# Kernel tuning notes

Measured on AMD Instinct MI355X. Metric: run time of the kernel, lower is better.

## Reference

```python
import jax, jax.numpy as jnp
import numpy as np
import math

MAX_DELAY = 25
TAU = 2.0
VTH = 1.0
BN_EPS = 1e-5
ATAN_ALPHA = 2.0


def build_dcls_kernel(W, P, SIG, D):
    # Gaussian-interpolated DCLS kernel ('gauss' version).
    # W, P, SIG: (O, I, K) -> kernel (O, I, D)
    lim = D // 2
    j = jnp.arange(D, dtype=W.dtype)                      # (D,)
    Pc = jnp.clip(P, -lim, lim) + lim                     # (O, I, K)
    sig = jnp.abs(SIG) + 0.27
    g = jnp.exp(-0.5 * ((j - Pc[..., None]) / sig[..., None]) ** 2)  # (O,I,K,D)
    g = g / (g.sum(-1, keepdims=True) + 1e-7)
    return jnp.einsum('oik,oikd->oid', W, g)


def dcls_conv_positive(x, W, P, SIG, D):
    # Dale-positive: abs(weight) before kernel construction; padding=0 (VALID)
    k = build_dcls_kernel(jnp.abs(W), P, SIG, D)
    return jax.lax.conv_general_dilated(
        x, k, window_strides=(1,), padding='VALID',
        dimension_numbers=('NCW', 'OIW', 'NCW'))


def batchnorm_m(x, gamma, beta):
    # spikingjelly layer.BatchNorm1d step_mode='m' on (T, B, C):
    # flattens (T*B) as batch, normalizes per channel (training-mode stats).
    mean = x.mean(axis=(0, 1))
    var = x.var(axis=(0, 1))
    return (x - mean) * jax.lax.rsqrt(var + BN_EPS) * gamma + beta


def lif_multistep(x_seq, tau, v_th):
    # LIFNode, decay_input=False, v_reset=0 (hard reset), detach_reset=True,
    # ATan surrogate. x_seq: (T, B, C).
    inv_tau = jnp.asarray(1.0 / tau, x_seq.dtype)
    def step(v, xt):
        v = v * (1.0 - inv_tau) + xt              # charge (decay_input=False)
        u = v - v_th
        sg = jnp.arctan(0.5 * math.pi * ATAN_ALPHA * u) / math.pi + 0.5
        hard = (u >= 0).astype(xt.dtype)
        spike = sg + jax.lax.stop_gradient(hard - sg)
        v = v * (1.0 - jax.lax.stop_gradient(spike))   # hard reset, detached
        return v, spike
    v0 = jnp.zeros(x_seq.shape[1:], x_seq.dtype)
    _, spikes = jax.lax.scan(step, v0, x_seq)
    return spikes


def setup_inputs() -> dict:
    key = jax.random.key(0)
    ks = jax.random.split(key, 8)
    B, C_in, T = 64, 700, 300
    n_out, n_inh, K = 256, 128, 1
    return {
        'x': jax.random.normal(ks[0], (B, C_in, T), jnp.float32),
        'W_inh': jax.random.normal(ks[1], (n_inh, C_in, K), jnp.float32),
        'P_inh': jax.random.normal(ks[2], (n_inh, C_in, K), jnp.float32),
        'SIG_inh': jax.random.uniform(ks[3], (n_inh, C_in, K), jnp.float32),
        'W_exc': jax.random.normal(ks[4], (n_out, C_in, K), jnp.float32),
        'P_exc': jax.random.normal(ks[5], (n_out, C_in, K), jnp.float32),
        'SIG_exc': jax.random.uniform(ks[6], (n_out, C_in, K), jnp.float32),
        'w_exc_inh': jax.random.uniform(ks[7], (n_out, n_inh), jnp.float32),
        'bn_gamma': jnp.ones((n_inh,), jnp.float32),
        'bn_beta': jnp.zeros((n_inh,), jnp.float32),
    }


def reference(x, W_inh, P_inh, SIG_inh, W_exc, P_exc, SIG_exc, w_exc_inh,
              bn_gamma, bn_beta):
    # inhibitory branch
    in_inhib = dcls_conv_positive(x, W_inh, P_inh, SIG_inh, MAX_DELAY)  # (B,Ci,T')
    in_inhib = jnp.transpose(in_inhib, (2, 0, 1))                       # (T',B,Ci)
    in_inhib = batchnorm_m(in_inhib, bn_gamma, bn_beta)
    spikes = lif_multistep(in_inhib, TAU, VTH)                          # (T',B,Ci)
    out_inhib = jnp.einsum('tbi,oi->tbo', spikes, -jnp.abs(w_exc_inh))
    out_inhib = jnp.transpose(out_inhib, (1, 2, 0))                     # (B,O,T')
    # excitatory branch
    excit = dcls_conv_positive(x, W_exc, P_exc, SIG_exc, MAX_DELAY)     # (B,O,T')
    return excit + out_inhib
```

## Files before the change

### kernel.cpp

```cpp
#include <hip/hip_runtime.h>
#include <math.h>

#define CI   700
#define TIN  300
#define DD   25
#define TOUT 276
#define BB   64
#define OINH 128
#define OEXC 256

#define TROWS 312
#define IPAD  704

typedef __attribute__((ext_vector_type(8))) short short8;
typedef __attribute__((ext_vector_type(4))) float f32x4;
typedef __attribute__((ext_vector_type(8))) unsigned short ushort8v;

static __device__ __forceinline__ unsigned short f2bf(float f) {
    unsigned int u = __float_as_uint(f);
    unsigned int r = (u + 0x7FFFu + ((u >> 16) & 1u)) >> 16;
    return (unsigned short)r;
}
static __device__ __forceinline__ float bf2f(unsigned short h) {
    return __uint_as_float(((unsigned int)h) << 16);
}

static __device__ __forceinline__ void gload_lds16(const void* g, void* l) {
    __builtin_amdgcn_global_load_lds(
        (const __attribute__((address_space(1))) unsigned int*)g,
        (__attribute__((address_space(3))) unsigned int*)l, 16, 0, 0);
}

__global__ void build_kt(const float* __restrict__ W, const float* __restrict__ P,
                         const float* __restrict__ SIG, float* __restrict__ kt, int O) {
    int n = blockIdx.x * 256 + threadIdx.x;
    if (n >= O * CI) return;
    int o = n % O;
    int i = n / O;
    float w   = fabsf(W[o * CI + i]);
    float p   = fminf(fmaxf(P[o * CI + i], -12.f), 12.f) + 12.f;
    float sig = fabsf(SIG[o * CI + i]) + 0.27f;
    float inv = 1.f / sig;
    float g[DD];
    float sum = 0.f;
#pragma unroll
    for (int d = 0; d < DD; ++d) {
        float e = ((float)d - p) * inv;
        g[d] = expf(-0.5f * e * e);
        sum += g[d];
    }
    float sc = w / (sum + 1e-7f);
#pragma unroll
    for (int d = 0; d < DD; ++d)
        kt[(i * DD + d) * O + o] = g[d] * sc;
}

__global__ void kexc_build(const float* __restrict__ W, const float* __restrict__ P,
                           const float* __restrict__ SIG, unsigned short* __restrict__ kb2) {
    int n = blockIdx.x * 256 + threadIdx.x;
    if (n >= OEXC * IPAD) return;
    int o = n / IPAD, ip = n % IPAD;
    if (ip >= CI) {
#pragma unroll
        for (int d = 0; d < DD; ++d)
            kb2[((size_t)d * OEXC + o) * IPAD + ip] = 0;
        return;
    }
    float w   = fabsf(W[o * CI + ip]);
    float p   = fminf(fmaxf(P[o * CI + ip], -12.f), 12.f) + 12.f;
    float sig = fabsf(SIG[o * CI + ip]) + 0.27f;
    float inv = 1.f / sig;
    float g[DD];
    float sum = 0.f;
#pragma unroll
    for (int d = 0; d < DD; ++d) {
        float e = ((float)d - p) * inv;
        g[d] = expf(-0.5f * e * e);
        sum += g[d];
    }
    float sc = w / (sum + 1e-7f);
#pragma unroll
    for (int d = 0; d < DD; ++d)
        kb2[((size_t)d * OEXC + o) * IPAD + ip] = f2bf(g[d] * sc);
}

__global__ void kinh_build(const float* __restrict__ W, const float* __restrict__ P,
                           const float* __restrict__ SIG,
                           unsigned short* __restrict__ kbh, unsigned short* __restrict__ kbl) {
    int n = blockIdx.x * 256 + threadIdx.x;
    if (n >= OINH * IPAD) return;
    int o = n / IPAD, ip = n % IPAD;
    if (ip >= CI) {
#pragma unroll
        for (int d = 0; d < DD; ++d) {
            kbh[((size_t)d * OINH + o) * IPAD + ip] = 0;
            kbl[((size_t)d * OINH + o) * IPAD + ip] = 0;
        }
        return;
    }
    float w   = fabsf(W[o * CI + ip]);
    float p   = fminf(fmaxf(P[o * CI + ip], -12.f), 12.f) + 12.f;
    float sig = fabsf(SIG[o * CI + ip]) + 0.27f;
    float inv = 1.f / sig;
    float g[DD];
    float sum = 0.f;
#pragma unroll
    for (int d = 0; d < DD; ++d) {
        float e = ((float)d - p) * inv;
        g[d] = expf(-0.5f * e * e);
        sum += g[d];
    }
    float sc = w / (sum + 1e-7f);
#pragma unroll
    for (int d = 0; d < DD; ++d) {
        float v = g[d] * sc;
        unsigned short h = f2bf(v);
        kbh[((size_t)d * OINH + o) * IPAD + ip] = h;
        kbl[((size_t)d * OINH + o) * IPAD + ip] = f2bf(v - bf2f(h));
    }
}

__global__ __launch_bounds__(256)
void xt_kernel(const float* __restrict__ x, unsigned short* __restrict__ xTh,
               unsigned short* __restrict__ xTl) {
    __shared__ float tile[64][65];
    const int tid = threadIdx.x;
    const int t0 = blockIdx.x * 64, i0 = blockIdx.y * 64, b = blockIdx.z;
#pragma unroll
    for (int s = 0; s < 16; ++s) {
        int f = s * 256 + tid;
        int tt = f & 63, ii = f >> 6;
        float v = 0.f;
        if (t0 + tt < TIN && i0 + ii < CI)
            v = x[((size_t)b * CI + i0 + ii) * TIN + t0 + tt];
        tile[tt][ii] = v;
    }
    __syncthreads();
#pragma unroll
    for (int s = 0; s < 2; ++s) {
        int f = s * 256 + tid;
        int tt = f >> 3, g = f & 7;
        if (t0 + tt < TROWS) {
            ushort8v vh, vl;
#pragma unroll
            for (int e = 0; e < 8; ++e) {
                float v = tile[tt][g * 8 + e];
                unsigned short h = f2bf(v);
                vh[e] = h;
                vl[e] = f2bf(v - bf2f(h));
            }
            size_t off = ((size_t)b * TROWS + t0 + tt) * IPAD + i0 + g * 8;
            *(ushort8v*)(xTh + off) = vh;
            if (xTl) *(ushort8v*)(xTl + off) = vl;
        }
    }
}

__global__ void wt_kernel(const float* __restrict__ w, float* __restrict__ wt) {
    int n = blockIdx.x * 256 + threadIdx.x;
    if (n >= OINH * OEXC) return;
    int o = n % OEXC, c = n / OEXC;
    wt[c * OEXC + o] = -fabsf(w[o * OINH + c]);
}

__global__ __launch_bounds__(256)
void conv_fused_v6(const unsigned short* __restrict__ xTh, const unsigned short* __restrict__ xTl,
                   const unsigned short* __restrict__ kb2,
                   const unsigned short* __restrict__ kbh, const unsigned short* __restrict__ kbl,
                   float* __restrict__ pexc0, float* __restrict__ pexc1,
                   float* __restrict__ pinh0, float* __restrict__ pinh1) {
    __shared__ unsigned short lds[16384];

    const int tid  = threadIdx.x;
    const int wave = tid >> 6;
    const int lane = tid & 63;
    const int wo   = wave & 1;
    const int wt2  = wave >> 1;
    const int wtb  = wt2 * 48;
    const int l15 = lane & 15, l4 = lane >> 4;
    const int tt   = blockIdx.x % 3;
    const int ksp  = blockIdx.x / 3;
    const int role = blockIdx.y;
    const int b    = blockIdx.z;
    const int t0   = tt * 96;
    const int icb  = ksp * 11;

    const int ld_r = lane >> 2;
    const int ld_c = (((lane & 3) ^ ((lane >> 3) & 3)) << 4);
    const int SA   = (l15 >> 1) & 3;

    const size_t xstride = (size_t)IPAD * 2;
    const char* xh_base = (const char*)xTh + ((size_t)b * TROWS + t0) * xstride;
    const char* xl_base = (const char*)xTl + ((size_t)b * TROWS + t0) * xstride;

    if (role < 2) {
        unsigned short* xs = lds;
        unsigned short* ks = lds + 4096;
        const int o0 = role * 128;
        const int o0w = o0 + wo * 64;

        f32x4 acc[4][3];
#pragma unroll
        for (int i = 0; i < 4; ++i)
#pragma unroll
            for (int j = 0; j < 3; ++j) acc[i][j] = (f32x4)0.f;

        for (int c = 0; c < 11; ++c) {
            const size_t cb = (size_t)(icb + c) * 64;
            __syncthreads();
            for (int j = wave; j < 8; j += 4)
                gload_lds16(xh_base + (size_t)(16 * j + ld_r) * xstride + cb + ld_c,
                            (char*)xs + j * 1024);
            {
                const char* kbase = (const char*)kb2 + (size_t)o0w * xstride + cb;
                char* kdst = (char*)(ks + (0 * 2 + wo) * 2048);
#pragma unroll
                for (int j = 0; j < 4; ++j)
                    gload_lds16(kbase + (size_t)(16 * j + ld_r) * xstride + ld_c,
                                kdst + j * 1024);
            }
            asm volatile("s_waitcnt vmcnt(0)" ::: "memory");
            __syncthreads();

            for (int d = 0; d < DD; ++d) {
                const int cur = d & 1;
                if (d < DD - 1) {
                    const char* kbase = (const char*)kb2 +
                        ((size_t)((d + 1) * OEXC) + o0w) * xstride + cb;
                    char* kdst = (char*)(ks + ((cur ^ 1) * 2 + wo) * 2048);
#pragma unroll
                    for (int j = 0; j < 4; ++j)
                        gload_lds16(kbase + (size_t)(16 * j + ld_r) * xstride + ld_c,
                                    kdst + j * 1024);
                }
                const char* kp = (const char*)(ks + (cur * 2 + wo) * 2048);
                short8 A[4];
#pragma unroll
                for (int i = 0; i < 4; ++i)
                    A[i] = *(const short8*)(kp + (i * 16 + l15) * 64 + ((l4 ^ SA) << 4));
#pragma unroll
                for (int j = 0; j < 3; ++j) {
                    const int tr = wtb + j * 16 + l15 + d;
                    short8 Bv = *(const short8*)((const char*)xs + tr * 64 +
                                                 ((l4 ^ ((tr >> 1) & 3)) << 4));
#pragma unroll
                    for (int i = 0; i < 4; ++i)
                        acc[i][j] = __builtin_amdgcn_mfma_f32_16x16x32_bf16(
                            A[i], Bv, acc[i][j], 0, 0, 0);
                }
                asm volatile("s_waitcnt vmcnt(0)" ::: "memory");
                __syncthreads();
            }
        }
        float* dst = ksp ? pexc1 : pexc0;
#pragma unroll
        for (int i = 0; i < 4; ++i)
#pragma unroll
            for (int j = 0; j < 3; ++j) {
                const int t = t0 + wtb + j * 16 + l15;
                if (t < TOUT) {
                    float* op = dst + ((size_t)b * OEXC + o0w + i * 16 + l4 * 4) * TOUT + t;
#pragma unroll
                    for (int r = 0; r < 4; ++r) op[(size_t)r * TOUT] = acc[i][j][r];
                }
            }
    } else {
        unsigned short* xsh = lds;
        unsigned short* xsl = lds + 4096;
        unsigned short* kws = lds + 8192;
        const int o0  = (role - 2) * 64;
        const int o0w = o0 + wo * 32;

        f32x4 acc[2][3];
#pragma unroll
        for (int i = 0; i < 2; ++i)
#pragma unroll
            for (int j = 0; j < 3; ++j) acc[i][j] = (f32x4)0.f;

        for (int c = 0; c < 11; ++c) {
            const size_t cb = (size_t)(icb + c) * 64;
            __syncthreads();
            for (int j = wave; j < 8; j += 4) {
                gload_lds16(xh_base + (size_t)(16 * j + ld_r) * xstride + cb + ld_c,
                            (char*)xsh + j * 1024);
                gload_lds16(xl_base + (size_t)(16 * j + ld_r) * xstride + cb + ld_c,
                            (char*)xsl + j * 1024);
            }
            {
                const size_t ko = (size_t)o0w * xstride + cb;
                char* kdst = (char*)(kws + (0 * 2 + wo) * 2048);
#pragma unroll
                for (int j = 0; j < 2; ++j) {
                    gload_lds16((const char*)kbh + ko + (size_t)(16 * j + ld_r) * xstride + ld_c,
                                kdst + j * 1024);
                    gload_lds16((const char*)kbl + ko + (size_t)(16 * j + ld_r) * xstride + ld_c,
                                kdst + 2048 + j * 1024);
                }
            }
            asm volatile("s_waitcnt vmcnt(0)" ::: "memory");
            __syncthreads();

            for (int d = 0; d < DD; ++d) {
                const int cur = d & 1;
                if (d < DD - 1) {
                    const size_t ko = ((size_t)((d + 1) * OINH) + o0w) * xstride + cb;
                    char* kdst = (char*)(kws + ((cur ^ 1) * 2 + wo) * 2048);
#pragma unroll
                    for (int j = 0; j < 2; ++j) {
                        gload_lds16((const char*)kbh + ko + (size_t)(16 * j + ld_r) * xstride + ld_c,
                                    kdst + j * 1024);
                        gload_lds16((const char*)kbl + ko + (size_t)(16 * j + ld_r) * xstride + ld_c,
                                    kdst + 2048 + j * 1024);
                    }
                }
                const char* kp = (const char*)(kws + (cur * 2 + wo) * 2048);
                short8 Ah[2], Al[2];
#pragma unroll
                for (int i = 0; i < 2; ++i) {
                    Ah[i] = *(const short8*)(kp + (i * 16 + l15) * 64 + ((l4 ^ SA) << 4));
                    Al[i] = *(const short8*)(kp + 2048 + (i * 16 + l15) * 64 + ((l4 ^ SA) << 4));
                }
#pragma unroll
                for (int j = 0; j < 3; ++j) {
                    const int tr = wtb + j * 16 + l15 + d;
                    const int xo = tr * 64 + ((l4 ^ ((tr >> 1) & 3)) << 4);
                    short8 Bh = *(const short8*)((const char*)xsh + xo);
                    short8 Bl = *(const short8*)((const char*)xsl + xo);
#pragma unroll
                    for (int i = 0; i < 2; ++i) {
                        acc[i][j] = __builtin_amdgcn_mfma_f32_16x16x32_bf16(
                            Ah[i], Bh, acc[i][j], 0, 0, 0);
                        acc[i][j] = __builtin_amdgcn_mfma_f32_16x16x32_bf16(
                            Ah[i], Bl, acc[i][j], 0, 0, 0);
                        acc[i][j] = __builtin_amdgcn_mfma_f32_16x16x32_bf16(
                            Al[i], Bh, acc[i][j], 0, 0, 0);
                    }
                }
                asm volatile("s_waitcnt vmcnt(0)" ::: "memory");
                __syncthreads();
            }
        }
        float* dst = ksp ? pinh1 : pinh0;
#pragma unroll
        for (int i = 0; i < 2; ++i)
#pragma unroll
            for (int j = 0; j < 3; ++j) {
                const int t = t0 + wtb + j * 16 + l15;
                if (t < TOUT) {
                    float* op = dst + ((size_t)b * OINH + o0w + i * 16 + l4 * 4) * TOUT + t;
#pragma unroll
                    for (int r = 0; r < 4; ++r) op[(size_t)r * TOUT] = acc[i][j][r];
                }
            }
    }
}

__global__ void add_exc(const float* __restrict__ p1, float* __restrict__ out) {
    int n = blockIdx.x * 256 + threadIdx.x;
    float4 a = ((const float4*)out)[n];
    float4 v = ((const float4*)p1)[n];
    a.x += v.x; a.y += v.y; a.z += v.z; a.w += v.w;
    ((float4*)out)[n] = a;
}

__global__ void bn_stats2(float* __restrict__ cinh, const float* __restrict__ q1,
                          const float* __restrict__ gamma, const float* __restrict__ beta,
                          float* __restrict__ scale, float* __restrict__ shift) {
    const int c = blockIdx.x, tid = threadIdx.x;
    float sum = 0.f, sq = 0.f;
    for (int idx = tid; idx < BB * TOUT; idx += 256) {
        int b = idx / TOUT, t = idx - b * TOUT;
        size_t off = (size_t)(b * OINH + c) * TOUT + t;
        float v = cinh[off] + q1[off];
        cinh[off] = v;
        sum += v; sq += v * v;
    }
#pragma unroll
    for (int off = 32; off; off >>= 1) {
        sum += __shfl_down(sum, off);
        sq  += __shfl_down(sq, off);
    }
    __shared__ float ls[8];
    int wid = tid >> 6;
    if ((tid & 63) == 0) { ls[wid * 2] = sum; ls[wid * 2 + 1] = sq; }
    __syncthreads();
    if (tid == 0) {
        float S = 0.f, Q = 0.f;
#pragma unroll
        for (int wv = 0; wv < 4; ++wv) { S += ls[wv * 2]; Q += ls[wv * 2 + 1]; }
        const float n = (float)(BB * TOUT);
        float mean = S / n;
        float var  = Q / n - mean * mean;
        float rs   = 1.f / sqrtf(var + 1e-5f);
        float sc   = gamma[c] * rs;
        scale[c] = sc;
        shift[c] = beta[c] - mean * sc;
    }
}

__global__ __launch_bounds__(128)
void lif2(const float* __restrict__ cinh, const float* __restrict__ scale,
          const float* __restrict__ shift, unsigned char* __restrict__ spk) {
    __shared__ float tile[128 * 65];
    const int b = blockIdx.x, c = threadIdx.x;
    const float sc = scale[c], sh = shift[c];
    const float* base = cinh + (size_t)b * OINH * TOUT;
    float v = 0.f;
    for (int tc = 0; tc < TOUT; tc += 64) {
        const int len = (TOUT - tc < 64) ? (TOUT - tc) : 64;
        const int L4 = len >> 2;
        __syncthreads();
        for (int q = c; q < 128 * L4; q += 128) {
            int cc = q / L4, e = q - cc * L4;
            float4 vv = *(const float4*)(base + (size_t)cc * TOUT + tc + e * 4);
            float* dstp = &tile[cc * 65 + e * 4];
            dstp[0] = vv.x; dstp[1] = vv.y; dstp[2] = vv.z; dstp[3] = vv.w;
        }
        __syncthreads();
        for (int t2 = 0; t2 < len; ++t2) {
            float xin = tile[c * 65 + t2] * sc + sh;
            v = 0.5f * v + xin;
            bool s = (v >= 1.f);
            spk[((size_t)(tc + t2) * BB + b) * OINH + c] = s ? 1 : 0;
            v = s ? 0.f : v;
        }
    }
}

__global__ __launch_bounds__(128)
void conv_mfma(const unsigned short* __restrict__ xTh, const unsigned short* __restrict__ kb2,
               float* __restrict__ out) {
    __shared__ unsigned short xs[120 * 64];
    __shared__ unsigned short ks[2][2][64 * 64];

    const int tid  = threadIdx.x;
    const int wave = tid >> 6;
    const int lane = tid & 63;
    const int l15 = lane & 15, l4 = lane >> 4, l7 = lane & 7;
    const int b  = blockIdx.z;
    const int t0 = blockIdx.x * 96;
    const int o0 = blockIdx.y * 128 + wave * 64;

    const int ld_row = lane >> 3;
    const int ld_swz = ((l7 ^ ld_row) << 4);

    f32x4 acc[4][6];
#pragma unroll
    for (int i = 0; i < 4; ++i)
#pragma unroll
        for (int j = 0; j < 6; ++j) acc[i][j] = (f32x4)0.f;

    const char* xrow0 = (const char*)xTh + ((size_t)b * TROWS + t0) * (IPAD * 2);

    for (int ic = 0; ic < 11; ++ic) {
        const int ic0 = ic * 64;
        __syncthreads();
        for (int j = wave; j < 15; j += 2)
            gload_lds16(xrow0 + (size_t)(8 * j + ld_row) * (IPAD * 2) + ic0 * 2 + ld_swz,
                        (char*)xs + j * 1024);
        {
            const char* ksrc = (const char*)kb2 + ((size_t)o0) * (IPAD * 2) + ic0 * 2;
            char* kdst = (char*)ks + (0 * 2 + wave) * 8192;
#pragma unroll
            for (int j = 0; j < 8; ++j)
                gload_lds16(ksrc + (size_t)(8 * j + ld_row) * (IPAD * 2) + ld_swz,
                            kdst + j * 1024);
        }
        asm volatile("s_waitcnt vmcnt(0)" ::: "memory");
        __syncthreads();

        for (int d = 0; d < DD; ++d) {
            const int cur = d & 1;
            if (d < DD - 1) {
                const char* ksrc = (const char*)kb2 +
                    ((size_t)(d + 1) * OEXC + o0) * (IPAD * 2) + ic0 * 2;
                char* kdst = (char*)ks + ((cur ^ 1) * 2 + wave) * 8192;
#pragma unroll
                for (int j = 0; j < 8; ++j)
                    gload_lds16(ksrc + (size_t)(8 * j + ld_row) * (IPAD * 2) + ld_swz,
                                kdst + j * 1024);
            }
            const char* kp = (const char*)ks + (cur * 2 + wave) * 8192;
#pragma unroll
            for (int ks2 = 0; ks2 < 2; ++ks2) {
                const int cg = ks2 * 4 + l4;
                short8 A[4];
#pragma unroll
                for (int i = 0; i < 4; ++i)
                    A[i] = *(const short8*)(kp + (i * 16 + l15) * 128 + ((cg ^ l7) << 4));
#pragma unroll
                for (int j = 0; j < 6; ++j) {
                    const int tr = j * 16 + l15 + d;
                    short8 Bv = *(const short8*)((const char*)xs + tr * 128 +
                                                 ((cg ^ (tr & 7)) << 4));
#pragma unroll
                    for (int i = 0; i < 4; ++i)
                        acc[i][j] = __builtin_amdgcn_mfma_f32_16x16x32_bf16(
                            A[i], Bv, acc[i][j], 0, 0, 0);
                }
            }
            asm volatile("s_waitcnt vmcnt(0)" ::: "memory");
        }
    }

#pragma unroll
    for (int i = 0; i < 4; ++i)
#pragma unroll
        for (int j = 0; j < 6; ++j) {
            const int tt = t0 + j * 16 + l15;
            if (tt < TOUT) {
                float* op = out + ((size_t)b * OEXC + o0 + i * 16 + l4 * 4) * TOUT + tt;
#pragma unroll
                for (int r = 0; r < 4; ++r) op[(size_t)r * TOUT] = acc[i][j][r];
            }
        }
}

__global__ __launch_bounds__(128)
void conv_mfma_inh(const unsigned short* __restrict__ xTh, const unsigned short* __restrict__ xTl,
                   const unsigned short* __restrict__ kbh, const unsigned short* __restrict__ kbl,
                   float* __restrict__ cinh) {
    __shared__ unsigned short xsh[120 * 64];
    __shared__ unsigned short xsl[120 * 64];
    __shared__ unsigned short ksh[2][64 * 64];
    __shared__ unsigned short ksl[2][64 * 64];

    const int tid  = threadIdx.x;
    const int wave = tid >> 6;
    const int lane = tid & 63;
    const int l15 = lane & 15, l4 = lane >> 4, l7 = lane & 7;
    const int b  = blockIdx.z;
    const int t0 = blockIdx.x * 96;
    const int o0 = blockIdx.y * 64;
    const int wtb = wave * 48;

    const int ld_row = lane >> 3;
    const int ld_swz = ((l7 ^ ld_row) << 4);

    f32x4 acc[4][3];
#pragma unroll
    for (int i = 0; i < 4; ++i)
#pragma unroll
        for (int j = 0; j < 3; ++j) acc[i][j] = (f32x4)0.f;

    const char* xrh = (const char*)xTh + ((size_t)b * TROWS + t0) * (IPAD * 2);
    const char* xrl = (const char*)xTl + ((size_t)b * TROWS + t0) * (IPAD * 2);
    const unsigned short* kb = wave ? kbl : kbh;

    for (int ic = 0; ic < 11; ++ic) {
        const int ic0 = ic * 64;
        __syncthreads();
        for (int j = wave; j < 15; j += 2) {
            gload_lds16(xrh + (size_t)(8 * j + ld_row) * (IPAD * 2) + ic0 * 2 + ld_swz,
                        (char*)xsh + j * 1024);
            gload_lds16(xrl + (size_t)(8 * j + ld_row) * (IPAD * 2) + ic0 * 2 + ld_swz,
                        (char*)xsl + j * 1024);
        }
        {
            char* kd = wave ? (char*)ksl[0] : (char*)ksh[0];
#pragma unroll
            for (int j = 0; j < 8; ++j)
                gload_lds16((const char*)kb +
                                ((size_t)(0 * OINH + o0 + 8 * j + ld_row)) * (IPAD * 2) +
                                ic0 * 2 + ld_swz,
                            kd + j * 1024);
        }
        asm volatile("s_waitcnt vmcnt(0)" ::: "memory");
        __syncthreads();

        for (int d = 0; d < DD; ++d) {
            const int cur = d & 1;
            if (d < DD - 1) {
                char* kd = wave ? (char*)ksl[cur ^ 1] : (char*)ksh[cur ^ 1];
#pragma unroll
                for (int j = 0; j < 8; ++j)
                    gload_lds16((const char*)kb +
                                    ((size_t)((d + 1) * OINH + o0 + 8 * j + ld_row)) * (IPAD * 2) +
                                    ic0 * 2 + ld_swz,
                                kd + j * 1024);
            }
            const char* kph = (const char*)ksh[cur];
            const char* kpl = (const char*)ksl[cur];
#pragma unroll
            for (int k2 = 0; k2 < 2; ++k2) {
                const int cg = k2 * 4 + l4;
                short8 Ah[4], Al[4];
#pragma unroll
                for (int i = 0; i < 4; ++i) {
                    Ah[i] = *(const short8*)(kph + (i * 16 + l15) * 128 + ((cg ^ l7) << 4));
                    Al[i] = *(const short8*)(kpl + (i * 16 + l15) * 128 + ((cg ^ l7) << 4));
                }
#pragma unroll
                for (int j = 0; j < 3; ++j) {
                    const int tr = wtb + j * 16 + l15 + d;
                    short8 Bh = *(const short8*)((const char*)xsh + tr * 128 +
                                                 ((cg ^ (tr & 7)) << 4));
                    short8 Bl = *(const short8*)((const char*)xsl + tr * 128 +
                                                 ((cg ^ (tr & 7)) << 4));
#pragma unroll
                    for (int i = 0; i < 4; ++i) {
                        acc[i][j] = __builtin_amdgcn_mfma_f32_16x16x32_bf16(
                            Ah[i], Bh, acc[i][j], 0, 0, 0);
                        acc[i][j] = __builtin_amdgcn_mfma_f32_16x16x32_bf16(
                            Ah[i], Bl, acc[i][j], 0, 0, 0);
                        acc[i][j] = __builtin_amdgcn_mfma_f32_16x16x32_bf16(
                            Al[i], Bh, acc[i][j], 0, 0, 0);
                    }
                }
            }
            asm volatile("s_waitcnt vmcnt(0)" ::: "memory");
            __syncthreads();
        }
    }

#pragma unroll
    for (int i = 0; i < 4; ++i)
#pragma unroll
        for (int j = 0; j < 3; ++j) {
            const int tt = t0 + wtb + j * 16 + l15;
            if (tt < TOUT) {
                float* op = cinh + ((size_t)b * OINH + o0 + i * 16 + l4 * 4) * TOUT + tt;
#pragma unroll
                for (int r = 0; r < 4; ++r) op[(size_t)r * TOUT] = acc[i][j][r];
            }
        }
}

__global__ __launch_bounds__(256)
void conv_dcls_fb(const float* __restrict__ x, const float* __restrict__ kt,
                  float* __restrict__ out, int O) {
    __shared__ float k_lds[100 * 128];
    __shared__ float x_lds[4 * 88];

    const int tid = threadIdx.x;
    const int tx = tid & 7;
    const int ty = tid >> 3;
    const int b  = blockIdx.z;
    const int t0 = blockIdx.x * 64;
    const int o0 = blockIdx.y * 128;
    const int tlim = TIN - t0;

    float acc[4][8];
#pragma unroll
    for (int ro = 0; ro < 4; ++ro)
#pragma unroll
        for (int rt = 0; rt < 8; ++rt) acc[ro][rt] = 0.f;

    for (int chunk = 0; chunk < 175; ++chunk) {
        const int i0 = chunk * 4;
        __syncthreads();
#pragma unroll
        for (int s = 0; s < 13; ++s) {
            int f = tid + s * 256;
            if (f < 3200) {
                int j = f >> 5, o4 = f & 31;
                ((float4*)k_lds)[f] =
                    *(const float4*)(kt + (size_t)(i0 * DD + j) * O + o0 + o4 * 4);
            }
        }
        if (tid < 88) {
            int icc = tid / 22, wq = tid % 22;
            float4 v = make_float4(0.f, 0.f, 0.f, 0.f);
            if (wq * 4 < tlim)
                v = *(const float4*)(x + (size_t)(b * CI + i0 + icc) * TIN + t0 + wq * 4);
            ((float4*)x_lds)[tid] = v;
        }
        __syncthreads();
#pragma unroll
        for (int icc = 0; icc < 4; ++icc) {
            float xv[32];
#pragma unroll
            for (int wq = 0; wq < 8; ++wq)
                *(float4*)(xv + 4 * wq) = ((const float4*)(x_lds + icc * 88))[tx * 2 + wq];
#pragma unroll
            for (int d = 0; d < DD; ++d) {
                float4 kv = ((const float4*)(k_lds + (icc * DD + d) * 128))[ty];
                float kvv[4] = {kv.x, kv.y, kv.z, kv.w};
#pragma unroll
                for (int ro = 0; ro < 4; ++ro)
#pragma unroll
                    for (int rt = 0; rt < 8; ++rt)
                        acc[ro][rt] += kvv[ro] * xv[rt + d];
            }
        }
    }
    const int tvalid = TOUT - t0;
#pragma unroll
    for (int ro = 0; ro < 4; ++ro) {
        float* op = out + (size_t)(b * O + o0 + ty * 4 + ro) * TOUT + t0;
#pragma unroll
        for (int u = 0; u < 2; ++u) {
            int toff = tx * 8 + u * 4;
            if (toff < tvalid) {
                float4 v = make_float4(acc[ro][u * 4 + 0], acc[ro][u * 4 + 1],
                                       acc[ro][u * 4 + 2], acc[ro][u * 4 + 3]);
                *(float4*)(op + toff) = v;
            }
        }
    }
}

__global__ void bn_stats(const float* __restrict__ cinh, const float* __restrict__ gamma,
                         const float* __restrict__ beta, float* __restrict__ scale,
                         float* __restrict__ shift) {
    const int c = blockIdx.x, tid = threadIdx.x;
    float sum = 0.f, sq = 0.f;
    for (int idx = tid; idx < BB * TOUT; idx += 256) {
        int b = idx / TOUT, t = idx - b * TOUT;
        float v = cinh[(size_t)(b * OINH + c) * TOUT + t];
        sum += v; sq += v * v;
    }
#pragma unroll
    for (int off = 32; off; off >>= 1) {
        sum += __shfl_down(sum, off);
        sq  += __shfl_down(sq, off);
    }
    __shared__ float ls[8];
    int wid = tid >> 6;
    if ((tid & 63) == 0) { ls[wid * 2] = sum; ls[wid * 2 + 1] = sq; }
    __syncthreads();
    if (tid == 0) {
        float S = 0.f, Q = 0.f;
#pragma unroll
        for (int wv = 0; wv < 4; ++wv) { S += ls[wv * 2]; Q += ls[wv * 2 + 1]; }
        const float n = (float)(BB * TOUT);
        float mean = S / n;
        float var  = Q / n - mean * mean;
        float rs   = 1.f / sqrtf(var + 1e-5f);
        float sc   = gamma[c] * rs;
        scale[c] = sc;
        shift[c] = beta[c] - mean * sc;
    }
}

__global__ void lif_kernel(const float* __restrict__ cinh, const float* __restrict__ scale,
                           const float* __restrict__ shift, unsigned char* __restrict__ spk) {
    const int b = blockIdx.x, c = threadIdx.x;
    const float sc = scale[c], sh = shift[c];
    const float* row = cinh + (size_t)(b * OINH + c) * TOUT;
    float v = 0.f;
    for (int t = 0; t < TOUT; ++t) {
        float xin = row[t] * sc + sh;
        v = 0.5f * v + xin;
        unsigned char s = (v >= 1.f) ? 1 : 0;
        spk[((size_t)t * BB + b) * OINH + c] = s;
        v = (v >= 1.f) ? 0.f : v;
    }
}

__global__ __launch_bounds__(256)
void finale(const unsigned char* __restrict__ spk, const float* __restrict__ wt,
            float* __restrict__ out) {
    __shared__ float s_lds[64 * 129];
    const int tid = threadIdx.x;
    const int tx = tid & 15, ty = tid >> 4;
    const int b = blockIdx.z, t0 = blockIdx.x * 64, o0 = blockIdx.y * 64;

#pragma unroll
    for (int s = 0; s < 32; ++s) {
        int f = tid + s * 256;
        int tt = f >> 7, c = f & 127;
        float v = 0.f;
        if (t0 + tt < TOUT) v = (float)spk[((size_t)(t0 + tt) * BB + b) * OINH + c];
        s_lds[tt * 129 + c] = v;
    }
    __syncthreads();

    float acc[4][4] = {{0.f}};
#pragma unroll 4
    for (int c = 0; c < 128; ++c) {
        float4 wv = *(const float4*)(wt + c * OEXC + o0 + ty * 4);
        float wvv[4] = {wv.x, wv.y, wv.z, wv.w};
        float sv[4];
#pragma unroll
        for (int rt = 0; rt < 4; ++rt) sv[rt] = s_lds[(tx * 4 + rt) * 129 + c];
#pragma unroll
        for (int ro = 0; ro < 4; ++ro)
#pragma unroll
            for (int rt = 0; rt < 4; ++rt)
                acc[ro][rt] += wvv[ro] * sv[rt];
    }

    const int tvalid = TOUT - t0;
    if (tx * 4 < tvalid) {
#pragma unroll
        for (int ro = 0; ro < 4; ++ro) {
            float* op = out + (size_t)(b * OEXC + o0 + ty * 4 + ro) * TOUT + t0 + tx * 4;
            float4 v = *(float4*)op;
            v.x += acc[ro][0]; v.y += acc[ro][1]; v.z += acc[ro][2]; v.w += acc[ro][3];
            *(float4*)op = v;
        }
    }
}

extern "C" void kernel_launch(void* const* d_in, const int* in_sizes, int n_in,
                              void* d_out, int out_size, void* d_ws, size_t ws_size,
                              hipStream_t stream) {
    const float* x       = (const float*)d_in[0];
    const float* W_inh   = (const float*)d_in[1];
    const float* P_inh   = (const float*)d_in[2];
    const float* SIG_inh = (const float*)d_in[3];
    const float* W_exc   = (const float*)d_in[4];
    const float* P_exc   = (const float*)d_in[5];
    const float* SIG_exc = (const float*)d_in[6];
    const float* w_ei    = (const float*)d_in[7];
    const float* gamma   = (const float*)d_in[8];
    const float* beta    = (const float*)d_in[9];
    float* out = (float*)d_out;

    const size_t XT_ELEMS   = (size_t)BB * TROWS * IPAD;
    const size_t KEXC_ELEMS = (size_t)DD * OEXC * IPAD;
    const size_t KINH_ELEMS = (size_t)DD * OINH * IPAD;
    const size_t CINH_ELEMS = (size_t)BB * OINH * TOUT;
    const size_t PEXC_ELEMS = (size_t)BB * OEXC * TOUT;

    const size_t NEED_FAST = 2 * XT_ELEMS * 2 + KEXC_ELEMS * 2 + 2 * KINH_ELEMS * 2 +
                             CINH_ELEMS * 4 + OINH * OEXC * 4 + CINH_ELEMS;
    const size_t NEED_FAST2 = (2 * XT_ELEMS + KEXC_ELEMS + 2 * KINH_ELEMS) * 2 +
                              (PEXC_ELEMS + 2 * CINH_ELEMS + OINH * OEXC + 256) * 4 +
                              CINH_ELEMS;

    if (ws_size >= NEED_FAST2) {
        unsigned short* xTh = (unsigned short*)d_ws;
        unsigned short* xTl = xTh + XT_ELEMS;
        unsigned short* kb2 = xTl + XT_ELEMS;
        unsigned short* kbh = kb2 + KEXC_ELEMS;
        unsigned short* kbl = kbh + KINH_ELEMS;
        float* pexc1 = (float*)(kbl + KINH_ELEMS);
        float* cinh  = pexc1 + PEXC_ELEMS;
        float* pinh1 = cinh + CINH_ELEMS;
        float* wt    = pinh1 + CINH_ELEMS;
        float* scale = wt + OINH * OEXC;
        float* shift = scale + OINH;
        unsigned char* spk = (unsigned char*)(shift + OINH);

        hipLaunchKernelGGL(kexc_build, dim3((OEXC * IPAD + 255) / 256), dim3(256), 0, stream,
                           W_exc, P_exc, SIG_exc, kb2);
        hipLaunchKernelGGL(kinh_build, dim3((OINH * IPAD + 255) / 256), dim3(256), 0, stream,
                           W_inh, P_inh, SIG_inh, kbh, kbl);
        hipLaunchKernelGGL(xt_kernel, dim3(5, 11, 64), dim3(256), 0, stream, x, xTh, xTl);
        hipLaunchKernelGGL(wt_kernel, dim3(128), dim3(256), 0, stream, w_ei, wt);

        hipLaunchKernelGGL(conv_fused_v6, dim3(6, 4, 64), dim3(256), 0, stream,
                           xTh, xTl, kb2, kbh, kbl, out, pexc1, cinh, pinh1);

        hipLaunchKernelGGL(add_exc, dim3((unsigned)(PEXC_ELEMS / 4 / 256)), dim3(256), 0, stream,
                           pexc1, out);
        hipLaunchKernelGGL(bn_stats2, dim3(128), dim3(256), 0, stream,
                           cinh, pinh1, gamma, beta, scale, shift);
        hipLaunchKernelGGL(lif2, dim3(64), dim3(128), 0, stream, cinh, scale, shift, spk);
        hipLaunchKernelGGL(finale, dim3(5, 4, 64), dim3(256), 0, stream, spk, wt, out);
    } else if (ws_size >= NEED_FAST) {
        unsigned short* xTh = (unsigned short*)d_ws;
        unsigned short* xTl = xTh + XT_ELEMS;
        unsigned short* kb2 = xTl + XT_ELEMS;
        unsigned short* kbh = kb2 + KEXC_ELEMS;
        unsigned short* kbl = kbh + KINH_ELEMS;
        float* cinh  = (float*)(kbl + KINH_ELEMS);
        float* wt    = cinh + CINH_ELEMS;
        float* scale = wt + OINH * OEXC;
        float* shift = scale + OINH;
        unsigned char* spk = (unsigned char*)(shift + OINH);

        hipLaunchKernelGGL(kexc_build, dim3((OEXC * IPAD + 255) / 256), dim3(256), 0, stream,
                           W_exc, P_exc, SIG_exc, kb2);
        hipLaunchKernelGGL(kinh_build, dim3((OINH * IPAD + 255) / 256), dim3(256), 0, stream,
                           W_inh, P_inh, SIG_inh, kbh, kbl);
        hipLaunchKernelGGL(xt_kernel, dim3(5, 11, 64), dim3(256), 0, stream, x, xTh, xTl);
        hipLaunchKernelGGL(wt_kernel, dim3(128), dim3(256), 0, stream, w_ei, wt);

        hipLaunchKernelGGL(conv_mfma, dim3(3, 2, 64), dim3(128), 0, stream, xTh, kb2, out);
        hipLaunchKernelGGL(conv_mfma_inh, dim3(3, 2, 64), dim3(128), 0, stream,
                           xTh, xTl, kbh, kbl, cinh);

        hipLaunchKernelGGL(bn_stats, dim3(128), dim3(256), 0, stream, cinh, gamma, beta, scale, shift);
        hipLaunchKernelGGL(lif_kernel, dim3(64), dim3(128), 0, stream, cinh, scale, shift, spk);
        hipLaunchKernelGGL(finale, dim3(5, 4, 64), dim3(256), 0, stream, spk, wt, out);
    } else {
        unsigned short* xTh = (unsigned short*)d_ws;
        unsigned short* kb2 = xTh + XT_ELEMS;
        float* kt_inh = (float*)(kb2 + KEXC_ELEMS);
        float* cinh   = kt_inh + 2240000;
        float* wt     = cinh + CINH_ELEMS;
        float* scale  = wt + OINH * OEXC;
        float* shift  = scale + OINH;
        unsigned char* spk = (unsigned char*)(shift + OINH);

        hipLaunchKernelGGL(kexc_build, dim3((OEXC * IPAD + 255) / 256), dim3(256), 0, stream,
                           W_exc, P_exc, SIG_exc, kb2);
        hipLaunchKernelGGL(build_kt, dim3(350), dim3(256), 0, stream,
                           W_inh, P_inh, SIG_inh, kt_inh, OINH);
        hipLaunchKernelGGL(xt_kernel, dim3(5, 11, 64), dim3(256), 0, stream, x, xTh,
                           (unsigned short*)nullptr);
        hipLaunchKernelGGL(wt_kernel, dim3(128), dim3(256), 0, stream, w_ei, wt);

        hipLaunchKernelGGL(conv_mfma, dim3(3, 2, 64), dim3(128), 0, stream, xTh, kb2, out);
        hipLaunchKernelGGL(conv_dcls_fb, dim3(5, 1, 64), dim3(256), 0, stream, x, kt_inh, cinh, OINH);

        hipLaunchKernelGGL(bn_stats, dim3(128), dim3(256), 0, stream, cinh, gamma, beta, scale, shift);
        hipLaunchKernelGGL(lif_kernel, dim3(64), dim3(128), 0, stream, cinh, scale, shift, spk);
        hipLaunchKernelGGL(finale, dim3(5, 4, 64), dim3(256), 0, stream, spk, wt, out);
    }
}
```

Baseline: 545.3 us.

## Process two batches per block to share kernel weight tiles across batches

The fused conv kernel now handles two batch elements per block. Each wave pair takes one batch and covers the full 96-row time tile, so every DCLS kernel tile loaded into LDS is reused for two batches and weight traffic is halved. The grid z dimension drops from 64 to 32, LDS grows to 48KB, and the accumulator count per wave doubles (24 tiles for exc), which raises register pressure. A launch bound of 3 blocks per CU is added to keep occupancy up.

Result: faster. 479.0 us (-12.2%).

```diff
diff --git a/kernel.cpp b/kernel.cpp
--- a/kernel.cpp
+++ b/kernel.cpp
@@ -163,25 +163,24 @@
     wt[c * OEXC + o] = -fabsf(w[o * OINH + c]);
 }
 
-__global__ __launch_bounds__(256)
-void conv_fused_v6(const unsigned short* __restrict__ xTh, const unsigned short* __restrict__ xTl,
+__global__ __launch_bounds__(256, 3)
+void conv_fused_v7(const unsigned short* __restrict__ xTh, const unsigned short* __restrict__ xTl,
                    const unsigned short* __restrict__ kb2,
                    const unsigned short* __restrict__ kbh, const unsigned short* __restrict__ kbl,
                    float* __restrict__ pexc0, float* __restrict__ pexc1,
                    float* __restrict__ pinh0, float* __restrict__ pinh1) {
-    __shared__ unsigned short lds[16384];
+    __shared__ unsigned short lds[24576];
 
     const int tid  = threadIdx.x;
     const int wave = tid >> 6;
     const int lane = tid & 63;
+    const int wb   = wave >> 1;
     const int wo   = wave & 1;
-    const int wt2  = wave >> 1;
-    const int wtb  = wt2 * 48;
     const int l15 = lane & 15, l4 = lane >> 4;
     const int tt   = blockIdx.x % 3;
     const int ksp  = blockIdx.x / 3;
     const int role = blockIdx.y;
-    const int b    = blockIdx.z;
+    const int bp   = blockIdx.z;
     const int t0   = tt * 96;
     const int icb  = ksp * 11;
 
@@ -190,30 +189,31 @@
     const int SA   = (l15 >> 1) & 3;
 
     const size_t xstride = (size_t)IPAD * 2;
-    const char* xh_base = (const char*)xTh + ((size_t)b * TROWS + t0) * xstride;
-    const char* xl_base = (const char*)xTl + ((size_t)b * TROWS + t0) * xstride;
 
     if (role < 2) {
-        unsigned short* xs = lds;
-        unsigned short* ks = lds + 4096;
-        const int o0 = role * 128;
+        const int o0  = role * 128;
         const int o0w = o0 + wo * 64;
-
-        f32x4 acc[4][3];
+        const int b   = 2 * bp + wb;
+
+        f32x4 acc[4][6];
 #pragma unroll
         for (int i = 0; i < 4; ++i)
 #pragma unroll
-            for (int j = 0; j < 3; ++j) acc[i][j] = (f32x4)0.f;
+            for (int j = 0; j < 6; ++j) acc[i][j] = (f32x4)0.f;
 
         for (int c = 0; c < 11; ++c) {
             const size_t cb = (size_t)(icb + c) * 64;
             __syncthreads();
-            for (int j = wave; j < 8; j += 4)
-                gload_lds16(xh_base + (size_t)(16 * j + ld_r) * xstride + cb + ld_c,
-                            (char*)xs + j * 1024);
+            for (int j = wave; j < 16; j += 4) {
+                const int q = j >> 3, jj = j & 7;
+                const char* xb = (const char*)xTh +
+                    ((size_t)(2 * bp + q) * TROWS + t0) * xstride;
+                gload_lds16(xb + (size_t)(16 * jj + ld_r) * xstride + cb + ld_c,
+                            (char*)lds + q * 8192 + jj * 1024);
+            }
             {
                 const char* kbase = (const char*)kb2 + (size_t)o0w * xstride + cb;
-                char* kdst = (char*)(ks + (0 * 2 + wo) * 2048);
+                char* kdst = (char*)lds + 16384 + (0 * 2 + wo) * 4096;
 #pragma unroll
                 for (int j = 0; j < 4; ++j)
                     gload_lds16(kbase + (size_t)(16 * j + ld_r) * xstride + ld_c,
@@ -227,21 +227,21 @@
                 if (d < DD - 1) {
                     const char* kbase = (const char*)kb2 +
                         ((size_t)((d + 1) * OEXC) + o0w) * xstride + cb;
-                    char* kdst = (char*)(ks + ((cur ^ 1) * 2 + wo) * 2048);
+                    char* kdst = (char*)lds + 16384 + ((cur ^ 1) * 2 + wo) * 4096;
 #pragma unroll
                     for (int j = 0; j < 4; ++j)
                         gload_lds16(kbase + (size_t)(16 * j + ld_r) * xstride + ld_c,
                                     kdst + j * 1024);
                 }
-                const char* kp = (const char*)(ks + (cur * 2 + wo) * 2048);
+                const char* kp = (const char*)lds + 16384 + (cur * 2 + wo) * 4096;
                 short8 A[4];
 #pragma unroll
                 for (int i = 0; i < 4; ++i)
                     A[i] = *(const short8*)(kp + (i * 16 + l15) * 64 + ((l4 ^ SA) << 4));
 #pragma unroll
-                for (int j = 0; j < 3; ++j) {
-                    const int tr = wtb + j * 16 + l15 + d;
-                    short8 Bv = *(const short8*)((const char*)xs + tr * 64 +
+                for (int j = 0; j < 6; ++j) {
+                    const int tr = j * 16 + l15 + d;
+                    short8 Bv = *(const short8*)((const char*)lds + wb * 8192 + tr * 64 +
                                                  ((l4 ^ ((tr >> 1) & 3)) << 4));
 #pragma unroll
                     for (int i = 0; i < 4; ++i)
@@ -256,8 +256,8 @@
 #pragma unroll
         for (int i = 0; i < 4; ++i)
 #pragma unroll
-            for (int j = 0; j < 3; ++j) {
-                const int t = t0 + wtb + j * 16 + l15;
+            for (int j = 0; j < 6; ++j) {
+                const int t = t0 + j * 16 + l15;
                 if (t < TOUT) {
                     float* op = dst + ((size_t)b * OEXC + o0w + i * 16 + l4 * 4) * TOUT + t;
 #pragma unroll
@@ -265,30 +265,31 @@
                 }
             }
     } else {
-        unsigned short* xsh = lds;
-        unsigned short* xsl = lds + 4096;
-        unsigned short* kws = lds + 8192;
         const int o0  = (role - 2) * 64;
         const int o0w = o0 + wo * 32;
-
-        f32x4 acc[2][3];
+        const int b   = 2 * bp + wb;
+
+        f32x4 acc[2][6];
 #pragma unroll
         for (int i = 0; i < 2; ++i)
 #pragma unroll
-            for (int j = 0; j < 3; ++j) acc[i][j] = (f32x4)0.f;
+            for (int j = 0; j < 6; ++j) acc[i][j] = (f32x4)0.f;
 
         for (int c = 0; c < 11; ++c) {
             const size_t cb = (size_t)(icb + c) * 64;
             __syncthreads();
-            for (int j = wave; j < 8; j += 4) {
-                gload_lds16(xh_base + (size_t)(16 * j + ld_r) * xstride + cb + ld_c,
-                            (char*)xsh + j * 1024);
-                gload_lds16(xl_base + (size_t)(16 * j + ld_r) * xstride + cb + ld_c,
-                            (char*)xsl + j * 1024);
+            for (int j = wave; j < 16; j += 4) {
+                const int q = j >> 3, jj = j & 7;
+                const size_t rowoff = ((size_t)(2 * bp + q) * TROWS + t0) * xstride +
+                                      (size_t)(16 * jj + ld_r) * xstride + cb + ld_c;
+                gload_lds16((const char*)xTh + rowoff,
+                            (char*)lds + q * 8192 + jj * 1024);
+                gload_lds16((const char*)xTl + rowoff,
+                            (char*)lds + 16384 + q * 8192 + jj * 1024);
             }
             {
                 const size_t ko = (size_t)o0w * xstride + cb;
-                char* kdst = (char*)(kws + (0 * 2 + wo) * 2048);
+                char* kdst = (char*)lds + 32768 + (0 * 2 + wo) * 4096;
 #pragma unroll
                 for (int j = 0; j < 2; ++j) {
                     gload_lds16((const char*)kbh + ko + (size_t)(16 * j + ld_r) * xstride + ld_c,
@@ -304,7 +305,7 @@
                 const int cur = d & 1;
                 if (d < DD - 1) {
                     const size_t ko = ((size_t)((d + 1) * OINH) + o0w) * xstride + cb;
-                    char* kdst = (char*)(kws + ((cur ^ 1) * 2 + wo) * 2048);
+                    char* kdst = (char*)lds + 32768 + ((cur ^ 1) * 2 + wo) * 4096;
 #pragma unroll
                     for (int j = 0; j < 2; ++j) {
                         gload_lds16((const char*)kbh + ko + (size_t)(16 * j + ld_r) * xstride + ld_c,
@@ -313,7 +314,7 @@
                                     kdst + 2048 + j * 1024);
                     }
                 }
-                const char* kp = (const char*)(kws + (cur * 2 + wo) * 2048);
+                const char* kp = (const char*)lds + 32768 + (cur * 2 + wo) * 4096;
                 short8 Ah[2], Al[2];
 #pragma unroll
                 for (int i = 0; i < 2; ++i) {
@@ -321,11 +322,11 @@
                     Al[i] = *(const short8*)(kp + 2048 + (i * 16 + l15) * 64 + ((l4 ^ SA) << 4));
                 }
 #pragma unroll
-                for (int j = 0; j < 3; ++j) {
-                    const int tr = wtb + j * 16 + l15 + d;
+                for (int j = 0; j < 6; ++j) {
+                    const int tr = j * 16 + l15 + d;
                     const int xo = tr * 64 + ((l4 ^ ((tr >> 1) & 3)) << 4);
-                    short8 Bh = *(const short8*)((const char*)xsh + xo);
-                    short8 Bl = *(const short8*)((const char*)xsl + xo);
+                    short8 Bh = *(const short8*)((const char*)lds + wb * 8192 + xo);
+                    short8 Bl = *(const short8*)((const char*)lds + 16384 + wb * 8192 + xo);
 #pragma unroll
                     for (int i = 0; i < 2; ++i) {
                         acc[i][j] = __builtin_amdgcn_mfma_f32_16x16x32_bf16(
@@ -344,8 +345,8 @@
 #pragma unroll
         for (int i = 0; i < 2; ++i)
 #pragma unroll
-            for (int j = 0; j < 3; ++j) {
-                const int t = t0 + wtb + j * 16 + l15;
+            for (int j = 0; j < 6; ++j) {
+                const int t = t0 + j * 16 + l15;
                 if (t < TOUT) {
                     float* op = dst + ((size_t)b * OINH + o0w + i * 16 + l4 * 4) * TOUT + t;
 #pragma unroll
@@ -841,7 +842,7 @@
         hipLaunchKernelGGL(xt_kernel, dim3(5, 11, 64), dim3(256), 0, stream, x, xTh, xTl);
         hipLaunchKernelGGL(wt_kernel, dim3(128), dim3(256), 0, stream, w_ei, wt);
 
-        hipLaunchKernelGGL(conv_fused_v6, dim3(6, 4, 64), dim3(256), 0, stream,
+        hipLaunchKernelGGL(conv_fused_v7, dim3(6, 4, 32), dim3(256), 0, stream,
                            xTh, xTl, kb2, kbh, kbl, out, pexc1, cinh, pinh1);
 
         hipLaunchKernelGGL(add_exc, dim3((unsigned)(PEXC_ELEMS / 4 / 256)), dim3(256), 0, stream,
```
